# Kernel optimization log

Measured on AMD Instinct MI355X. Metric: run time of the kernel, lower is better.

Reference implementation:

```python
import jax, jax.numpy as jnp
import numpy as np

B, N, C, H, I, ID = 4, 1024, 1024, 16, 77, 768
HD = C // H
HID = 4 * C


def _ln(t, w, b):
    m = jnp.mean(t, axis=-1, keepdims=True)
    v = jnp.mean((t - m) ** 2, axis=-1, keepdims=True)
    return (t - m) * jax.lax.rsqrt(v + 1e-5) * w + b


def _gelu(t):
    return jax.nn.gelu(t, approximate=False)


def setup_inputs() -> dict:
    key = jax.random.key(0)
    ks = iter(jax.random.split(key, 16))

    def nrm(shape, s=0.02):
        return jax.random.normal(next(ks), shape, jnp.float32) * s

    return {
        'x': jax.random.normal(next(ks), (B, N, C), jnp.float32),
        'instruct_states': jax.random.normal(next(ks), (B, I, ID), jnp.float32),
        'norm1_w': jnp.ones((C,), jnp.float32), 'norm1_b': jnp.zeros((C,), jnp.float32),
        'qkv_w': nrm((3 * C, C)),
        'q_bias': jnp.zeros((C,), jnp.float32), 'v_bias': jnp.zeros((C,), jnp.float32),
        'proj_w': nrm((C, C)), 'proj_b': jnp.zeros((C,), jnp.float32),
        'gamma_1': jnp.full((C,), 1e-5, jnp.float32), 'gamma_2': jnp.full((C,), 1e-5, jnp.float32),
        'norm2_w': jnp.ones((C,), jnp.float32), 'norm2_b': jnp.zeros((C,), jnp.float32),
        'fc1_w': nrm((HID, C)), 'fc1_b': jnp.zeros((HID,), jnp.float32),
        'fc2_w': nrm((C, HID)), 'fc2_b': jnp.zeros((C,), jnp.float32),
        'pfc1_w': nrm((HID, C)), 'pfc1_b': jnp.zeros((HID,), jnp.float32),
        'pfc2_w': nrm((C, HID)), 'pfc2_b': jnp.zeros((C,), jnp.float32),
        'parallel_gate': jnp.full((1,), 0.1, jnp.float32),
        'ir_ln_w': jnp.ones((ID,), jnp.float32), 'ir_ln_b': jnp.zeros((ID,), jnp.float32),
        'ir_l1_w': nrm((C, ID)), 'ir_l1_b': jnp.zeros((C,), jnp.float32),
        'ir_l2_w': nrm((C, C)), 'ir_l2_b': jnp.zeros((C,), jnp.float32),
    }


def reference(x, instruct_states, norm1_w, norm1_b, qkv_w, q_bias, v_bias,
              proj_w, proj_b, gamma_1, gamma_2, norm2_w, norm2_b,
              fc1_w, fc1_b, fc2_w, fc2_b, pfc1_w, pfc1_b, pfc2_w, pfc2_b,
              parallel_gate, ir_ln_w, ir_ln_b, ir_l1_w, ir_l1_b, ir_l2_w, ir_l2_b):
    # instruct_dim_reduce: LN -> Linear -> GELU -> Linear
    kv = _ln(instruct_states, ir_ln_w, ir_ln_b)
    kv = _gelu(kv @ ir_l1_w.T + ir_l1_b) @ ir_l2_w.T + ir_l2_b  # [B, I, C]

    xn = _ln(x, norm1_w, norm1_b)                               # [B, N, C]
    cat = jnp.concatenate([kv, xn], axis=1)                     # [B, I+N, C]
    S = I + N

    qkv_bias = jnp.concatenate([q_bias, jnp.zeros_like(v_bias), v_bias])
    qkv = (cat @ qkv_w.T + qkv_bias).reshape(B, S, 3, H, HD)
    q = qkv[:, :, 0].transpose(0, 2, 1, 3)                      # [B, H, S, HD]
    k = qkv[:, :, 1].transpose(0, 2, 1, 3)
    v = qkv[:, :, 2].transpose(0, 2, 1, 3)

    # only visual queries, keys/values over instructions + visual tokens
    q = q[:, :, I:, :] * (HD ** -0.5)                           # [B, H, N, HD]
    attn = jnp.einsum('bhqd,bhkd->bhqk', q, k)                  # [B, H, N, S]
    attn = jax.nn.softmax(attn, axis=-1)
    o = jnp.einsum('bhqk,bhkd->bqhd', attn, v).reshape(B, N, C)
    o = o @ proj_w.T + proj_b

    x = x + gamma_1 * o                                         # LayerScale residual

    y = _ln(x, norm2_w, norm2_b)
    mlp = _gelu(y @ fc1_w.T + fc1_b) @ fc2_w.T + fc2_b
    pmlp = _gelu(y @ pfc1_w.T + pfc1_b) @ pfc2_w.T + pfc2_b
    x = x + gamma_2 * mlp + parallel_gate * pmlp
    return x
```

## Files before the change

### kernel.cpp

```cpp
#include <hip/hip_runtime.h>
#include <cstdint>

#define Bv   4
#define Nv   1024
#define Cv   1024
#define Hv   16
#define Iv   77
#define IDv  768
#define HDv  64
#define HIDv 4096
#define Sv   (Iv + Nv)
#define BIv  (Bv * Iv)
#define BSv  (Bv * Sv)
#define BNv  (Bv * Nv)
#define SPADv 1152

typedef __bf16 bf16x8_t __attribute__((ext_vector_type(8)));
typedef float  f32x4_t  __attribute__((ext_vector_type(4)));
typedef unsigned short us8_t __attribute__((ext_vector_type(8)));
typedef long  l2_t  __attribute__((ext_vector_type(2)));
typedef int   i32x4_t __attribute__((ext_vector_type(4)));
typedef int   i32x8_t __attribute__((ext_vector_type(8)));

__device__ inline f32x4_t zero4() { f32x4_t z; z[0]=0.f; z[1]=0.f; z[2]=0.f; z[3]=0.f; return z; }

__device__ inline unsigned short f2bf(float f) {
    unsigned int u = __builtin_bit_cast(unsigned int, f);
    u = (u + 0x7fffu + ((u >> 16) & 1u)) >> 16;
    return (unsigned short)u;
}
__device__ inline float bf2f(unsigned short u) {
    return __builtin_bit_cast(float, ((unsigned int)u) << 16);
}
__device__ inline unsigned int f4_fp8(float a, float b, float c, float d) {
    int v = __builtin_amdgcn_cvt_pk_fp8_f32(a, b, 0, false);
    v = __builtin_amdgcn_cvt_pk_fp8_f32(c, d, v, true);
    return (unsigned int)v;
}

__device__ inline float gelu_f(float x) {
    float u = 0.7978845608f * x * (1.0f + 0.044715f * x * x);
    float e = __expf(2.0f * u);
    float t = 1.0f - 2.0f / (e + 1.0f);
    return 0.5f * x * (1.0f + t);
}

__device__ inline void gload_lds16(const void* g, void* l) {
    __builtin_amdgcn_global_load_lds(
        (__attribute__((address_space(1))) void*)(unsigned long long)g,
        (__attribute__((address_space(3))) void*)(unsigned long long)l,
        16, 0, 0);
}

__device__ inline i32x8_t frag32(const unsigned char* p0, const unsigned char* p1) {
    i32x4_t lo = *(const i32x4_t*)p0;
    i32x4_t hi = *(const i32x4_t*)p1;
    i32x8_t r;
    r[0] = lo[0]; r[1] = lo[1]; r[2] = lo[2]; r[3] = lo[3];
    r[4] = hi[0]; r[5] = hi[1]; r[6] = hi[2]; r[7] = hi[3];
    return r;
}

#define PIPE_WAIT(N) do { \
    asm volatile("s_waitcnt vmcnt(" #N ")" ::: "memory"); \
    __builtin_amdgcn_s_barrier(); \
    __builtin_amdgcn_sched_barrier(0); \
} while (0)
#define PIPE_RELEASE() do { \
    __builtin_amdgcn_sched_barrier(0); \
    __builtin_amdgcn_s_barrier(); \
} while (0)

__global__ __launch_bounds__(256) void cvt8_kernel(
        const float* s0, const float* s1, const float* s2, const float* s3,
        const float* s4, const float* s5, const float* s6, const float* s7,
        void* d0, void* d1, void* d2, void* d3,
        void* d4, void* d5, void* d6, void* d7,
        const float* g1, const float* g2, const float* gate) {
    (void)g1;
    long i = (long)blockIdx.x * 256 + threadIdx.x;
    const float* src; void* dst; long off;
    const float* sptr = nullptr; int K4 = 1; float wmul = 1.0f; bool f8 = false;
    if (i < 2097152) {
        if (i < 786432)       { src = s0; dst = d0; off = i; f8 = true; wmul = 32.f; }
        else if (i < 1048576) { src = s1; dst = d1; off = i - 786432;  f8 = true; wmul = 32.f; }
        else                  { src = s2; dst = d2; off = i - 1048576; f8 = true; wmul = 32.f; }
    } else if (i < 4194304) {
        if (i < 3145728)      { src = s3; dst = d3; off = i - 2097152; f8 = true; wmul = 32.f; sptr = g2; K4 = 1024; }
        else                  { src = s4; dst = d4; off = i - 3145728; f8 = true; wmul = 32.f; }
    } else {
        if (i < 5242880)      { src = s5; dst = d5; off = i - 4194304; f8 = true; wmul = 32.f; sptr = gate; K4 = 0x7fffffff; }
        else if (i < 5439488) { src = s6; dst = d6; off = i - 5242880; }
        else                  { src = s7; dst = d7; off = i - 5439488; }
    }
    float sc = (sptr ? sptr[(int)(off / K4)] : 1.0f) * wmul;
    float4 v = ((const float4*)src)[off];
    if (f8) {
        ((unsigned int*)dst)[off] = f4_fp8(v.x * sc, v.y * sc, v.z * sc, v.w * sc);
    } else {
        ushort4 o = {f2bf(v.x * sc), f2bf(v.y * sc), f2bf(v.z * sc), f2bf(v.w * sc)};
        ((ushort4*)dst)[off] = o;
    }
}

__global__ __launch_bounds__(256) void bias_prep_kernel(
        const float* __restrict__ qb, const float* __restrict__ vb,
        const float* __restrict__ fc2b, const float* __restrict__ pfc2b,
        const float* __restrict__ projb_in,
        const float* __restrict__ fc1b, const float* __restrict__ pfc1b,
        const float* __restrict__ g1, const float* __restrict__ g2,
        const float* __restrict__ gate,
        float* __restrict__ qkvb, float* __restrict__ bfuse,
        float* __restrict__ projb, float* __restrict__ bcat) {
    int i = blockIdx.x * 256 + threadIdx.x;
    if (i < 3 * Cv) {
        float v = 0.f;
        if (i < Cv) v = qb[i];
        else if (i >= 2 * Cv) v = vb[i - 2 * Cv];
        qkvb[i] = v;
    } else if (i < 4 * Cv) {
        int n = i - 3 * Cv;
        bfuse[n] = g2[n] * fc2b[n] + gate[0] * pfc2b[n];
    } else if (i < 5 * Cv) {
        int n = i - 4 * Cv;
        projb[n] = g1[n] * projb_in[n];
    } else if (i < 13 * Cv) {
        int j = i - 5 * Cv;
        bcat[j] = (j < HIDv) ? fc1b[j] : pfc1b[j - HIDv];
    }
}

__global__ __launch_bounds__(256) void scatter_kv_kernel(const unsigned short* __restrict__ kv,
                                                         unsigned char* __restrict__ cat) {
    int r = blockIdx.x;
    int b = r / Iv, i = r % Iv;
    const ushort4* src = (const ushort4*)(kv + (size_t)r * Cv);
    unsigned int* dst = (unsigned int*)(cat + (size_t)(b * Sv + i) * Cv);
    ushort4 u = src[threadIdx.x];
    dst[threadIdx.x] = f4_fp8(bf2f(u.x) * 16.f, bf2f(u.y) * 16.f,
                              bf2f(u.z) * 16.f, bf2f(u.w) * 16.f);
}

template <int F8>
__global__ __launch_bounds__(256) void ln_kernel(const float* __restrict__ in,
                                                 const float* __restrict__ w,
                                                 const float* __restrict__ bvec,
                                                 void* __restrict__ out,
                                                 int cols, float invcols,
                                                 int div_, int stride_, int off_) {
    const int r = blockIdx.x;
    const int tid = threadIdx.x;
    const float* row = in + (size_t)r * cols;
    float s = 0.f, s2 = 0.f;
    for (int c = tid * 4; c < cols; c += 1024) {
        float4 v = *(const float4*)(row + c);
        s  += v.x + v.y + v.z + v.w;
        s2 += v.x * v.x + v.y * v.y + v.z * v.z + v.w * v.w;
    }
#pragma unroll
    for (int o2 = 32; o2 > 0; o2 >>= 1) { s += __shfl_down(s, o2); s2 += __shfl_down(s2, o2); }
    __shared__ float sh[10];
    const int lane = tid & 63, wave = tid >> 6;
    if (lane == 0) { sh[wave] = s; sh[4 + wave] = s2; }
    __syncthreads();
    if (tid == 0) {
        float S1 = sh[0] + sh[1] + sh[2] + sh[3];
        float S2 = sh[4] + sh[5] + sh[6] + sh[7];
        float mean = S1 * invcols;
        float var  = S2 * invcols - mean * mean;
        sh[8] = mean;
        sh[9] = rsqrtf(var + 1e-5f);
    }
    __syncthreads();
    const float mean = sh[8], rstd = sh[9];
    const size_t orow = (size_t)((r / div_) * stride_ + (r % div_) + off_) * cols;
    for (int c = tid * 4; c < cols; c += 1024) {
        float4 v  = *(const float4*)(row + c);
        float4 wv = *(const float4*)(w + c);
        float4 bv = *(const float4*)(bvec + c);
        float o0 = (v.x - mean) * rstd * wv.x + bv.x;
        float o1 = (v.y - mean) * rstd * wv.y + bv.y;
        float o2 = (v.z - mean) * rstd * wv.z + bv.z;
        float o3 = (v.w - mean) * rstd * wv.w + bv.w;
        if constexpr (F8) {
            *(unsigned int*)((unsigned char*)out + orow + c) =
                f4_fp8(o0 * 16.f, o1 * 16.f, o2 * 16.f, o3 * 16.f);
        } else {
            ushort4 o = {f2bf(o0), f2bf(o1), f2bf(o2), f2bf(o3)};
            *(ushort4*)((unsigned short*)out + orow + c) = o;
        }
    }
}

template <int MODE>
__global__ __launch_bounds__(256) void gemm_bf16_kernel(
        const unsigned short* __restrict__ A,
        const unsigned short* __restrict__ W,
        const float* __restrict__ bias,
        unsigned short* __restrict__ outp,
        int M, int N, int K) {
    __shared__ unsigned short As[2][128 * 32];
    __shared__ unsigned short Bs[2][128 * 32];
    const int tid  = threadIdx.x;
    const int lane = tid & 63;
    const int wave = tid >> 6;
    const int m16  = lane & 15;
    const int g4   = lane >> 4;
    const int n0 = blockIdx.x * 128;
    const int m0 = blockIdx.y * 128;
    const int wm = (wave >> 1) * 64;
    const int wn = (wave & 1) * 64;

    const int r0  = tid >> 2;
    const int cc0 = (tid & 3) * 8;
    int am0 = m0 + r0;       if (am0 > M - 1) am0 = M - 1;
    int am1 = m0 + r0 + 64;  if (am1 > M - 1) am1 = M - 1;
    const unsigned short* agp0 = A + (size_t)am0 * K + cc0;
    const unsigned short* agp1 = A + (size_t)am1 * K + cc0;
    const unsigned short* bgp0 = W + (size_t)(n0 + r0) * K + cc0;
    const unsigned short* bgp1 = W + (size_t)(n0 + r0 + 64) * K + cc0;

    f32x4_t acc[4][4];
#pragma unroll
    for (int a = 0; a < 4; ++a)
#pragma unroll
        for (int bb = 0; bb < 4; ++bb) acc[a][bb] = zero4();

    auto stage = [&](int buf) {
        gload_lds16(agp0, &As[buf][wave * 512]);
        gload_lds16(agp1, &As[buf][2048 + wave * 512]);
        gload_lds16(bgp0, &Bs[buf][wave * 512]);
        gload_lds16(bgp1, &Bs[buf][2048 + wave * 512]);
        agp0 += 32; agp1 += 32; bgp0 += 32; bgp1 += 32;
    };

    auto body = [&](int cur) {
        bf16x8_t xf[4], wf[4];
#pragma unroll
        for (int bb = 0; bb < 4; ++bb)
            xf[bb] = *(const bf16x8_t*)&As[cur][(wm + bb * 16 + m16) * 32 + g4 * 8];
#pragma unroll
        for (int a = 0; a < 4; ++a)
            wf[a] = *(const bf16x8_t*)&Bs[cur][(wn + a * 16 + m16) * 32 + g4 * 8];
#pragma unroll
        for (int a = 0; a < 4; ++a)
#pragma unroll
            for (int bb = 0; bb < 4; ++bb)
                acc[a][bb] = __builtin_amdgcn_mfma_f32_16x16x32_bf16(wf[a], xf[bb], acc[a][bb], 0, 0, 0);
    };

    const int NIT = K >> 5;
    stage(0);
    stage(1);
    for (int it = 0; it < NIT - 1; ++it) {
        const int cur = it & 1;
        PIPE_WAIT(4);
        body(cur);
        PIPE_RELEASE();
        if (it + 2 < NIT) stage(cur);
    }
    PIPE_WAIT(0);
    body((NIT - 1) & 1);

#pragma unroll
    for (int a = 0; a < 4; ++a) {
        const int cb = n0 + wn + a * 16 + g4 * 4;
        const float4 bv4 = *(const float4*)(bias + cb);
#pragma unroll
        for (int bb = 0; bb < 4; ++bb) {
            const int r = m0 + wm + bb * 16 + m16;
            if (r < M) {
                const size_t idx = (size_t)r * N + cb;
                const float v0 = acc[a][bb][0] + bv4.x;
                const float v1 = acc[a][bb][1] + bv4.y;
                const float v2 = acc[a][bb][2] + bv4.z;
                const float v3 = acc[a][bb][3] + bv4.w;
                if constexpr (MODE == 0) {
                    ushort4 o = {f2bf(v0), f2bf(v1), f2bf(v2), f2bf(v3)};
                    *(ushort4*)(outp + idx) = o;
                } else {
                    ushort4 o = {f2bf(gelu_f(v0)), f2bf(gelu_f(v1)),
                                 f2bf(gelu_f(v2)), f2bf(gelu_f(v3))};
                    *(ushort4*)(outp + idx) = o;
                }
            }
        }
    }
}

__global__ __launch_bounds__(256) void gemm_fp8_bf16out_kernel(
        const unsigned char* __restrict__ A,
        const unsigned char* __restrict__ W,
        const float* __restrict__ bias,
        unsigned short* __restrict__ outp,
        int M, int N, int K) {
    __shared__ unsigned char As[2][128 * 128];
    __shared__ unsigned char Bs[2][128 * 128];
    const int tid  = threadIdx.x;
    const int lane = tid & 63;
    const int wave = tid >> 6;
    const int m16  = lane & 15;
    const int g4   = lane >> 4;
    const int n0 = blockIdx.x * 128;
    const int m0 = blockIdx.y * 128;
    const int wm = (wave >> 1) * 64;
    const int wn = (wave & 1) * 64;

    const int rowin = tid >> 3;
    const int sslot = (tid & 7) ^ (rowin & 7);
    const unsigned char* agp[4];
#pragma unroll
    for (int j = 0; j < 4; ++j) {
        int gr = m0 + j * 32 + rowin; if (gr > M - 1) gr = M - 1;
        agp[j] = A + (size_t)gr * K + sslot * 16;
    }
    const unsigned char* bgp = W + (size_t)(n0 + rowin) * K + sslot * 16;

    const int sw = m16 & 7;
    const int ra0 = ((2 * g4) ^ sw) * 16;
    const int ra1 = ((2 * g4 + 1) ^ sw) * 16;

    f32x4_t acc[4][4];
#pragma unroll
    for (int a = 0; a < 4; ++a)
#pragma unroll
        for (int bb = 0; bb < 4; ++bb) acc[a][bb] = zero4();

    auto stage = [&](int buf) {
#pragma unroll
        for (int j = 0; j < 4; ++j) {
            gload_lds16(agp[j], &As[buf][j * 4096 + wave * 1024]);
            gload_lds16(bgp + (size_t)j * 32 * K, &Bs[buf][j * 4096 + wave * 1024]);
            agp[j] += 128;
        }
        bgp += 128;
    };

    stage(0);
    const int NIT = K >> 7;
    for (int it = 0; it < NIT; ++it) {
        const int cur = it & 1;
        __syncthreads();
        if (it + 1 < NIT) stage(cur ^ 1);
        i32x8_t xv[4], wv[4];
#pragma unroll
        for (int bb = 0; bb < 4; ++bb) {
            const unsigned char* rb = &As[cur][(wm + bb * 16 + m16) * 128];
            xv[bb] = frag32(rb + ra0, rb + ra1);
        }
#pragma unroll
        for (int a = 0; a < 4; ++a) {
            const unsigned char* rb = &Bs[cur][(wn + a * 16 + m16) * 128];
            wv[a] = frag32(rb + ra0, rb + ra1);
        }
#pragma unroll
        for (int a = 0; a < 4; ++a)
#pragma unroll
            for (int bb = 0; bb < 4; ++bb)
                acc[a][bb] = __builtin_amdgcn_mfma_scale_f32_16x16x128_f8f6f4(
                    wv[a], xv[bb], acc[a][bb], 0, 0, 0, 0x7f7f7f7f, 0, 0x7f7f7f7f);
    }

    const float ds = 1.0f / 512.0f;
#pragma unroll
    for (int a = 0; a < 4; ++a) {
        const int cb = n0 + wn + a * 16 + g4 * 4;
        const float4 bv4 = *(const float4*)(bias + cb);
#pragma unroll
        for (int bb = 0; bb < 4; ++bb) {
            const int r = m0 + wm + bb * 16 + m16;
            if (r < M) {
                const size_t idx = (size_t)r * N + cb;
                ushort4 o = {f2bf(acc[a][bb][0] * ds + bv4.x),
                             f2bf(acc[a][bb][1] * ds + bv4.y),
                             f2bf(acc[a][bb][2] * ds + bv4.z),
                             f2bf(acc[a][bb][3] * ds + bv4.w)};
                *(ushort4*)(outp + idx) = o;
            }
        }
    }
}

__global__ __launch_bounds__(256) void gemm_fp8_gelu_kernel(
        const unsigned char* __restrict__ A,
        const unsigned char* __restrict__ W,
        const float* __restrict__ bias,
        unsigned char* __restrict__ outp,
        int M, int N, int K) {
    __shared__ unsigned char As[2][128 * 128];
    __shared__ unsigned char Bs[2][128 * 128];
    const int tid  = threadIdx.x;
    const int lane = tid & 63;
    const int wave = tid >> 6;
    const int m16  = lane & 15;
    const int g4   = lane >> 4;
    const int bid = blockIdx.x;
    const int xcd = bid & 7, l = bid >> 3;
    const int by = (xcd << 2) | (l & 3);
    const int bx = l >> 2;
    const int n0 = bx * 128;
    const int m0 = by * 128;
    const int wm = (wave >> 1) * 64;
    const int wn = (wave & 1) * 64;

    const int rowin = tid >> 3;
    const int sslot = (tid & 7) ^ (rowin & 7);
    const unsigned char* agp = A + (size_t)(m0 + rowin) * K + sslot * 16;
    const unsigned char* bgp = W + (size_t)(n0 + rowin) * K + sslot * 16;

    const int sw = m16 & 7;
    const int ra0 = ((2 * g4) ^ sw) * 16;
    const int ra1 = ((2 * g4 + 1) ^ sw) * 16;

    f32x4_t acc[4][4];
#pragma unroll
    for (int a = 0; a < 4; ++a)
#pragma unroll
        for (int bb = 0; bb < 4; ++bb) acc[a][bb] = zero4();

    auto stage = [&](int buf) {
#pragma unroll
        for (int j = 0; j < 4; ++j) {
            gload_lds16(agp + (size_t)j * 32 * K, &As[buf][j * 4096 + wave * 1024]);
            gload_lds16(bgp + (size_t)j * 32 * K, &Bs[buf][j * 4096 + wave * 1024]);
        }
        agp += 128; bgp += 128;
    };

    stage(0);
    const int NIT = K >> 7;
    for (int it = 0; it < NIT; ++it) {
        const int cur = it & 1;
        __syncthreads();
        if (it + 1 < NIT) stage(cur ^ 1);
        i32x8_t xv[4], wv[4];
#pragma unroll
        for (int bb = 0; bb < 4; ++bb) {
            const unsigned char* rb = &As[cur][(wm + bb * 16 + m16) * 128];
            xv[bb] = frag32(rb + ra0, rb + ra1);
        }
#pragma unroll
        for (int a = 0; a < 4; ++a) {
            const unsigned char* rb = &Bs[cur][(wn + a * 16 + m16) * 128];
            wv[a] = frag32(rb + ra0, rb + ra1);
        }
#pragma unroll
        for (int a = 0; a < 4; ++a)
#pragma unroll
            for (int bb = 0; bb < 4; ++bb)
                acc[a][bb] = __builtin_amdgcn_mfma_scale_f32_16x16x128_f8f6f4(
                    wv[a], xv[bb], acc[a][bb], 0, 0, 0, 0x7f7f7f7f, 0, 0x7f7f7f7f);
    }

    const float ds = 1.0f / 512.0f;
#pragma unroll
    for (int a = 0; a < 4; ++a) {
        const int cb = n0 + wn + a * 16 + g4 * 4;
        const float4 bv4 = *(const float4*)(bias + cb);
#pragma unroll
        for (int bb = 0; bb < 4; ++bb) {
            const int r = m0 + wm + bb * 16 + m16;
            const size_t idx = (size_t)r * N + cb;
            unsigned int pk = f4_fp8(gelu_f(acc[a][bb][0] * ds + bv4.x) * 16.f,
                                     gelu_f(acc[a][bb][1] * ds + bv4.y) * 16.f,
                                     gelu_f(acc[a][bb][2] * ds + bv4.z) * 16.f,
                                     gelu_f(acc[a][bb][3] * ds + bv4.w) * 16.f);
            *(unsigned int*)(outp + idx) = pk;
        }
    }
}

__global__ __launch_bounds__(256) void gemm_fp8_splitk_kernel(
        const unsigned char* __restrict__ A1,
        const unsigned char* __restrict__ W1,
        const unsigned char* __restrict__ A2,
        const unsigned char* __restrict__ W2,
        unsigned short* __restrict__ parts,
        int M, int N, int lda, int ldw, int Kc, int zsplit) {
    __shared__ unsigned char As[2][128 * 128];
    __shared__ unsigned char Bs[2][128 * 128];
    const int tid  = threadIdx.x;
    const int lane = tid & 63;
    const int wave = tid >> 6;
    const int m16  = lane & 15;
    const int g4   = lane >> 4;
    const int bid = blockIdx.x;
    const int xcd = bid & 7, l = bid >> 3;
    const int by = (xcd << 2) | (l & 3);
    const int rr = l >> 2;
    const int bx = rr & 7;
    const int z  = rr >> 3;
    const int n0 = bx * 128;
    const int m0 = by * 128;
    const int wm = (wave >> 1) * 64;
    const int wn = (wave & 1) * 64;

    const unsigned char* A = (z < zsplit) ? A1 : A2;
    const unsigned char* W = (z < zsplit) ? W1 : W2;
    const int k0 = (z % zsplit) * Kc;

    const int rowin = tid >> 3;
    const int sslot = (tid & 7) ^ (rowin & 7);
    const unsigned char* agp = A + (size_t)(m0 + rowin) * lda + k0 + sslot * 16;
    const unsigned char* bgp = W + (size_t)(n0 + rowin) * ldw + k0 + sslot * 16;

    const int sw = m16 & 7;
    const int ra0 = ((2 * g4) ^ sw) * 16;
    const int ra1 = ((2 * g4 + 1) ^ sw) * 16;

    f32x4_t acc[4][4];
#pragma unroll
    for (int a = 0; a < 4; ++a)
#pragma unroll
        for (int bb = 0; bb < 4; ++bb) acc[a][bb] = zero4();

    auto stage = [&](int buf) {
#pragma unroll
        for (int j = 0; j < 4; ++j) {
            gload_lds16(agp + (size_t)j * 32 * lda, &As[buf][j * 4096 + wave * 1024]);
            gload_lds16(bgp + (size_t)j * 32 * ldw, &Bs[buf][j * 4096 + wave * 1024]);
        }
        agp += 128; bgp += 128;
    };

    stage(0);
    const int NIT = Kc >> 7;
    for (int it = 0; it < NIT; ++it) {
        const int cur = it & 1;
        __syncthreads();
        if (it + 1 < NIT) stage(cur ^ 1);
        i32x8_t xv[4], wv[4];
#pragma unroll
        for (int bb = 0; bb < 4; ++bb) {
            const unsigned char* rb = &As[cur][(wm + bb * 16 + m16) * 128];
            xv[bb] = frag32(rb + ra0, rb + ra1);
        }
#pragma unroll
        for (int a = 0; a < 4; ++a) {
            const unsigned char* rb = &Bs[cur][(wn + a * 16 + m16) * 128];
            wv[a] = frag32(rb + ra0, rb + ra1);
        }
#pragma unroll
        for (int a = 0; a < 4; ++a)
#pragma unroll
            for (int bb = 0; bb < 4; ++bb)
                acc[a][bb] = __builtin_amdgcn_mfma_scale_f32_16x16x128_f8f6f4(
                    wv[a], xv[bb], acc[a][bb], 0, 0, 0, 0x7f7f7f7f, 0, 0x7f7f7f7f);
    }

    unsigned short* pz = parts + (size_t)z * M * N;
    const float ds = 1.0f / 512.0f;
#pragma unroll
    for (int a = 0; a < 4; ++a) {
        const int cb = n0 + wn + a * 16 + g4 * 4;
#pragma unroll
        for (int bb = 0; bb < 4; ++bb) {
            const int r = m0 + wm + bb * 16 + m16;
            const size_t idx = (size_t)r * N + cb;
            ushort4 o = {f2bf(acc[a][bb][0] * ds), f2bf(acc[a][bb][1] * ds),
                         f2bf(acc[a][bb][2] * ds), f2bf(acc[a][bb][3] * ds)};
            *(ushort4*)(pz + idx) = o;
        }
    }
}

template <int NP>
__global__ __launch_bounds__(256) void reduce_kernel(
        const unsigned short* __restrict__ parts,
        const float* __restrict__ resid,
        const float* __restrict__ bias,
        float* __restrict__ out, int MN, int N4mask) {
    int i = blockIdx.x * 256 + threadIdx.x;
    if (i * 4 >= MN) return;
    float4 res = ((const float4*)resid)[i];
    float4 bv  = *(const float4*)(bias + (i & N4mask) * 4);
    float4 o = {res.x + bv.x, res.y + bv.y, res.z + bv.z, res.w + bv.w};
#pragma unroll
    for (int z = 0; z < NP; ++z) {
        ushort4 u = ((const ushort4*)(parts + (size_t)z * MN))[i];
        o.x += bf2f(u.x); o.y += bf2f(u.y); o.z += bf2f(u.z); o.w += bf2f(u.w);
    }
    ((float4*)out)[i] = o;
}

template <int NP>
__global__ __launch_bounds__(256) void reduce_scale_kernel(
        const unsigned short* __restrict__ parts,
        const float* __restrict__ resid,
        const float* __restrict__ bias,
        const float* __restrict__ scale,
        float* __restrict__ out, int MN, int N4mask) {
    int i = blockIdx.x * 256 + threadIdx.x;
    if (i * 4 >= MN) return;
    float4 res = ((const float4*)resid)[i];
    const int c4 = (i & N4mask) * 4;
    float4 bv = *(const float4*)(bias + c4);
    float4 sc = *(const float4*)(scale + c4);
    float sx = 0.f, sy = 0.f, sz = 0.f, sw = 0.f;
#pragma unroll
    for (int z = 0; z < NP; ++z) {
        ushort4 u = ((const ushort4*)(parts + (size_t)z * MN))[i];
        sx += bf2f(u.x); sy += bf2f(u.y); sz += bf2f(u.z); sw += bf2f(u.w);
    }
    float4 o = {res.x + bv.x + sc.x * sx, res.y + bv.y + sc.y * sy,
                res.z + bv.z + sc.z * sz, res.w + bv.w + sc.w * sw};
    ((float4*)out)[i] = o;
}

__global__ __launch_bounds__(256) void vtrans_kernel(const unsigned short* __restrict__ qkv,
                                                     unsigned short* __restrict__ vt) {
    __shared__ unsigned short Vs[64 * 64];
    const int stile = blockIdx.x;
    const int bh = blockIdx.y;
    const int b = bh >> 4, h = bh & 15;
    const int tid = threadIdx.x;
#pragma unroll
    for (int j = 0; j < 2; ++j) {
        int c = j * 256 + tid;
        int r = c >> 3, d8 = (c & 7) * 8;
        int s = stile * 64 + r;
        uint4 v = {0u, 0u, 0u, 0u};
        if (s < Sv) v = *(const uint4*)(qkv + ((size_t)(b * Sv + s) * 3 + 2) * Cv + h * 64 + d8);
        *(uint4*)&Vs[r * 64 + d8] = v;
    }
    __syncthreads();
    const int d  = tid >> 2;
    const int p0 = (tid & 3) * 16;
    unsigned short tmp[16];
#pragma unroll
    for (int e = 0; e < 16; ++e) {
        int p = p0 + e;
        int s_local = (p & 32) + 16 * ((p >> 2) & 1) + 4 * ((p & 31) >> 3) + (p & 3);
        tmp[e] = Vs[s_local * 64 + d];
    }
    unsigned short* dst = vt + ((size_t)bh * 64 + d) * SPADv + stile * 64 + p0;
    *(uint4*)dst       = *(const uint4*)&tmp[0];
    *(uint4*)(dst + 8) = *(const uint4*)&tmp[8];
}

__global__ __launch_bounds__(256) void attn_kernel(const unsigned short* __restrict__ qkv,
                                                   const unsigned short* __restrict__ vt,
                                                   unsigned char* __restrict__ o) {
    __shared__ unsigned short Qs[64 * 64];
    __shared__ unsigned short Ks[2][64 * 64];
    __shared__ unsigned short Vts[2][64 * 64];

    const int tid  = threadIdx.x;
    const int lane = tid & 63;
    const int wave = tid >> 6;
    const int m16  = lane & 15;
    const int g4   = lane >> 4;
    const int qt = blockIdx.x;
    const int bh = blockIdx.y;
    const int b = bh >> 4, h = bh & 15;

    const int lr = lane >> 3;
    const int csw = ((lane & 7) ^ lr) * 8;
    const int sw7 = m16 & 7;

#pragma unroll
    for (int j = 0; j < 2; ++j) {
        int r = wave * 16 + j * 8 + lr;
        int s = Iv + qt * 64 + r;
        gload_lds16(qkv + ((size_t)(b * Sv + s) * 3) * Cv + h * 64 + csw,
                    &Qs[(wave * 16 + j * 8) * 64]);
    }

    auto stage_kv = [&](int st, int buf) {
#pragma unroll
        for (int j = 0; j < 2; ++j) {
            int r = wave * 16 + j * 8 + lr;
            int s = st * 64 + r; if (s > Sv - 1) s = Sv - 1;
            gload_lds16(qkv + ((size_t)(b * Sv + s) * 3 + 1) * Cv + h * 64 + csw,
                        &Ks[buf][(wave * 16 + j * 8) * 64]);
            gload_lds16(vt + ((size_t)bh * 64 + r) * SPADv + st * 64 + csw,
                        &Vts[buf][(wave * 16 + j * 8) * 64]);
        }
    };

    f32x4_t oacc[4];
#pragma unroll
    for (int dt = 0; dt < 4; ++dt) oacc[dt] = zero4();
    float m_run = -1e30f, l_run = 0.f;

    stage_kv(0, 0);
    __syncthreads();

    const bf16x8_t qf0 = *(const bf16x8_t*)&Qs[(wave * 16 + m16) * 64 + ((g4 ^ sw7) * 8)];
    const bf16x8_t qf1 = *(const bf16x8_t*)&Qs[(wave * 16 + m16) * 64 + (((4 + g4) ^ sw7) * 8)];

    const int NT = (Sv + 63) / 64;
    for (int st = 0; st < NT; ++st) {
        const int cur = st & 1;
        if (st + 1 < NT) stage_kv(st + 1, cur ^ 1);

        f32x4_t sc[4];
#pragma unroll
        for (int kt = 0; kt < 4; ++kt) {
            bf16x8_t k0 = *(const bf16x8_t*)&Ks[cur][(kt * 16 + m16) * 64 + ((g4 ^ sw7) * 8)];
            bf16x8_t k1 = *(const bf16x8_t*)&Ks[cur][(kt * 16 + m16) * 64 + (((4 + g4) ^ sw7) * 8)];
            f32x4_t z = zero4();
            z = __builtin_amdgcn_mfma_f32_16x16x32_bf16(k0, qf0, z, 0, 0, 0);
            z = __builtin_amdgcn_mfma_f32_16x16x32_bf16(k1, qf1, z, 0, 0, 0);
            sc[kt] = z;
        }

        float mx = -1e30f;
#pragma unroll
        for (int kt = 0; kt < 4; ++kt)
#pragma unroll
            for (int r = 0; r < 4; ++r) {
                int key = st * 64 + kt * 16 + g4 * 4 + r;
                float v = sc[kt][r] * 0.125f;
                v = (key < Sv) ? v : -1e30f;
                sc[kt][r] = v;
                mx = fmaxf(mx, v);
            }
        mx = fmaxf(mx, __shfl_xor(mx, 16));
        mx = fmaxf(mx, __shfl_xor(mx, 32));
        const float mnew  = fmaxf(m_run, mx);
        const float alpha = __expf(m_run - mnew);
        m_run = mnew;
        float sum = 0.f;
#pragma unroll
        for (int kt = 0; kt < 4; ++kt)
#pragma unroll
            for (int r = 0; r < 4; ++r) {
                float p = __expf(sc[kt][r] - mnew);
                sc[kt][r] = p;
                sum += p;
            }
        sum += __shfl_xor(sum, 16);
        sum += __shfl_xor(sum, 32);
        l_run = l_run * alpha + sum;
#pragma unroll
        for (int dt = 0; dt < 4; ++dt) oacc[dt] *= alpha;

        us8_t pu0, pu1;
#pragma unroll
        for (int j = 0; j < 8; ++j) {
            pu0[j] = f2bf(sc[(j >> 2)][j & 3]);
            pu1[j] = f2bf(sc[2 + (j >> 2)][j & 3]);
        }
        const bf16x8_t pf0 = __builtin_bit_cast(bf16x8_t, pu0);
        const bf16x8_t pf1 = __builtin_bit_cast(bf16x8_t, pu1);

#pragma unroll
        for (int dt = 0; dt < 4; ++dt) {
            bf16x8_t v0 = *(const bf16x8_t*)&Vts[cur][(dt * 16 + m16) * 64 + ((g4 ^ sw7) * 8)];
            bf16x8_t v1 = *(const bf16x8_t*)&Vts[cur][(dt * 16 + m16) * 64 + (((4 + g4) ^ sw7) * 8)];
            oacc[dt] = __builtin_amdgcn_mfma_f32_16x16x32_bf16(v0, pf0, oacc[dt], 0, 0, 0);
            oacc[dt] = __builtin_amdgcn_mfma_f32_16x16x32_bf16(v1, pf1, oacc[dt], 0, 0, 0);
        }
        __syncthreads();
    }

    const float inv16 = 16.0f / l_run;
    const int q = qt * 64 + wave * 16 + m16;
    const size_t row = (size_t)(b * Nv + q) * Cv + h * 64;
#pragma unroll
    for (int dt = 0; dt < 4; ++dt) {
        *(unsigned int*)&o[row + dt * 16 + g4 * 4] =
            f4_fp8(oacc[dt][0] * inv16, oacc[dt][1] * inv16,
                   oacc[dt][2] * inv16, oacc[dt][3] * inv16);
    }
}

extern "C" void kernel_launch(void* const* d_in, const int* in_sizes, int n_in,
                              void* d_out, int out_size, void* d_ws, size_t ws_size,
                              hipStream_t stream) {
    (void)in_sizes; (void)n_in; (void)out_size; (void)ws_size;
    const float* x       = (const float*)d_in[0];
    const float* instr   = (const float*)d_in[1];
    const float* norm1_w = (const float*)d_in[2];
    const float* norm1_b = (const float*)d_in[3];
    const float* qkv_w   = (const float*)d_in[4];
    const float* q_bias  = (const float*)d_in[5];
    const float* v_bias  = (const float*)d_in[6];
    const float* proj_w  = (const float*)d_in[7];
    const float* proj_b  = (const float*)d_in[8];
    const float* gamma_1 = (const float*)d_in[9];
    const float* gamma_2 = (const float*)d_in[10];
    const float* norm2_w = (const float*)d_in[11];
    const float* norm2_b = (const float*)d_in[12];
    const float* fc1_w   = (const float*)d_in[13];
    const float* fc1_b   = (const float*)d_in[14];
    const float* fc2_w   = (const float*)d_in[15];
    const float* fc2_b   = (const float*)d_in[16];
    const float* pfc1_w  = (const float*)d_in[17];
    const float* pfc1_b  = (const float*)d_in[18];
    const float* pfc2_w  = (const float*)d_in[19];
    const float* pfc2_b  = (const float*)d_in[20];
    const float* gate    = (const float*)d_in[21];
    const float* ir_ln_w = (const float*)d_in[22];
    const float* ir_ln_b = (const float*)d_in[23];
    const float* ir_l1_w = (const float*)d_in[24];
    const float* ir_l1_b = (const float*)d_in[25];
    const float* ir_l2_w = (const float*)d_in[26];
    const float* ir_l2_b = (const float*)d_in[27];
    float* out = (float*)d_out;

    char* ws = (char*)d_ws;
    size_t off = 0;
    auto alloc = [&](size_t bytes) -> char* {
        char* p = ws + off;
        off += (bytes + 255) & ~(size_t)255;
        return p;
    };
    unsigned char*  w_qkv8 = (unsigned char*)alloc((size_t)3 * Cv * Cv);
    unsigned char*  w_proj8= (unsigned char*)alloc((size_t)Cv * Cv);
    unsigned char*  w_mlp1 = (unsigned char*)alloc((size_t)2 * HIDv * Cv);
    unsigned char*  w_fc2  = (unsigned char*)alloc((size_t)Cv * HIDv);
    unsigned char*  w_pfc2 = (unsigned char*)alloc((size_t)Cv * HIDv);
    unsigned short* w_ir1  = (unsigned short*)alloc((size_t)Cv * IDv * 2);
    unsigned short* w_ir2  = (unsigned short*)alloc((size_t)Cv * Cv * 2);
    float*          qkvb   = (float*)alloc((size_t)3 * Cv * 4);
    float*          bfuse  = (float*)alloc((size_t)Cv * 4);
    float*          projb  = (float*)alloc((size_t)Cv * 4);
    float*          bcat   = (float*)alloc((size_t)2 * HIDv * 4);
    unsigned short* irln   = (unsigned short*)alloc((size_t)BIv * IDv * 2);
    unsigned short* h1     = (unsigned short*)alloc((size_t)BIv * Cv * 2);
    unsigned short* kvtmp  = (unsigned short*)alloc((size_t)BIv * Cv * 2);
    unsigned char*  cat8   = (unsigned char*)alloc((size_t)BSv * Cv);
    unsigned short* qkvbuf = (unsigned short*)alloc((size_t)BSv * 3 * Cv * 2);
    unsigned char*  obuf8  = (unsigned char*)alloc((size_t)BNv * Cv);
    float*          x1     = (float*)alloc((size_t)BNv * Cv * 4);
    unsigned char*  ybuf8  = (unsigned char*)alloc((size_t)BNv * Cv);
    unsigned char*  gbufA  = (unsigned char*)alloc((size_t)BNv * 2 * HIDv);
    unsigned short* fpart  = (unsigned short*)alloc((size_t)4 * BNv * Cv * 2);
    unsigned short* vt     = (unsigned short*)gbufA;
    unsigned short* ppart  = fpart;

    cvt8_kernel<<<22272, 256, 0, stream>>>(qkv_w, proj_w, fc1_w, fc2_w, pfc1_w, pfc2_w,
                                           ir_l1_w, ir_l2_w,
                                           w_qkv8, w_proj8, w_mlp1, w_fc2,
                                           w_mlp1 + (size_t)HIDv * Cv, w_pfc2,
                                           w_ir1, w_ir2,
                                           gamma_1, gamma_2, gate);

    bias_prep_kernel<<<52, 256, 0, stream>>>(q_bias, v_bias, fc2_b, pfc2_b, proj_b,
                                             fc1_b, pfc1_b,
                                             gamma_1, gamma_2, gate,
                                             qkvb, bfuse, projb, bcat);

    ln_kernel<0><<<BIv, 256, 0, stream>>>(instr, ir_ln_w, ir_ln_b, irln,
                                          IDv, 1.0f / IDv, 1 << 28, 0, 0);
    ln_kernel<1><<<BNv, 256, 0, stream>>>(x, norm1_w, norm1_b, cat8,
                                          Cv, 1.0f / Cv, Nv, Sv, Iv);
    gemm_bf16_kernel<1><<<dim3(Cv / 128, (BIv + 127) / 128), 256, 0, stream>>>(
        irln, w_ir1, ir_l1_b, h1, BIv, Cv, IDv);
    gemm_bf16_kernel<0><<<dim3(Cv / 128, (BIv + 127) / 128), 256, 0, stream>>>(
        h1, w_ir2, ir_l2_b, kvtmp, BIv, Cv, Cv);
    scatter_kv_kernel<<<BIv, 256, 0, stream>>>(kvtmp, cat8);

    gemm_fp8_bf16out_kernel<<<dim3(3 * Cv / 128, (BSv + 127) / 128), 256, 0, stream>>>(
        cat8, w_qkv8, qkvb, qkvbuf, BSv, 3 * Cv, Cv);

    vtrans_kernel<<<dim3(18, Bv * Hv), 256, 0, stream>>>(qkvbuf, vt);
    attn_kernel<<<dim3(Nv / 64, Bv * Hv), 256, 0, stream>>>(qkvbuf, vt, obuf8);

    gemm_fp8_splitk_kernel<<<1024, 256, 0, stream>>>(
        obuf8, w_proj8, obuf8, w_proj8, ppart,
        BNv, Cv, Cv, Cv, Cv / 4, 4);
    reduce_scale_kernel<4><<<(BNv * Cv / 4 + 255) / 256, 256, 0, stream>>>(
        ppart, x, projb, gamma_1, x1, BNv * Cv, Cv / 4 - 1);

    ln_kernel<1><<<BNv, 256, 0, stream>>>(x1, norm2_w, norm2_b, ybuf8,
                                          Cv, 1.0f / Cv, 1 << 28, 0, 0);

    gemm_fp8_gelu_kernel<<<2048, 256, 0, stream>>>(
        ybuf8, w_mlp1, bcat, gbufA, BNv, 2 * HIDv, Cv);

    gemm_fp8_splitk_kernel<<<1024, 256, 0, stream>>>(
        gbufA, w_fc2, gbufA + HIDv, w_pfc2, fpart,
        BNv, Cv, 2 * HIDv, HIDv, HIDv / 2, 2);
    reduce_kernel<4><<<(BNv * Cv / 4 + 255) / 256, 256, 0, stream>>>(
        fpart, x1, bfuse, out, BNv * Cv, Cv / 4 - 1);
}
```

Before: 436.8 us.

## Fuse proj reduce with LN2, fold kv scatter into GEMM, halve split-K

A new kernel combines the proj split-K partial reduction, residual add and the second LayerNorm into one pass. It writes x1 in fp32 and y in fp8 together, so x1 is no longer re-read from global memory. The instruct-reduce second GEMM gains an epilogue mode that writes fp8 rows straight into the concatenated buffer, which removes the temporary buffer and the scatter kernel. Split-K counts drop from 4 to 2 for both the proj and fc2 GEMMs, with half the launched blocks, which cuts partial-sum traffic but may lower parallelism. The LN variance now uses E[x²]-mean², which is less numerically stable.

```diff
diff --git a/kernel.cpp b/kernel.cpp
--- a/kernel.cpp
+++ b/kernel.cpp
@@ -130,17 +130,6 @@
     }
 }
 
-__global__ __launch_bounds__(256) void scatter_kv_kernel(const unsigned short* __restrict__ kv,
-                                                         unsigned char* __restrict__ cat) {
-    int r = blockIdx.x;
-    int b = r / Iv, i = r % Iv;
-    const ushort4* src = (const ushort4*)(kv + (size_t)r * Cv);
-    unsigned int* dst = (unsigned int*)(cat + (size_t)(b * Sv + i) * Cv);
-    ushort4 u = src[threadIdx.x];
-    dst[threadIdx.x] = f4_fp8(bf2f(u.x) * 16.f, bf2f(u.y) * 16.f,
-                              bf2f(u.z) * 16.f, bf2f(u.w) * 16.f);
-}
-
 template <int F8>
 __global__ __launch_bounds__(256) void ln_kernel(const float* __restrict__ in,
                                                  const float* __restrict__ w,
@@ -190,6 +179,56 @@
             *(ushort4*)((unsigned short*)out + orow + c) = o;
         }
     }
+}
+
+__global__ __launch_bounds__(256) void proj_ln2_kernel(
+        const unsigned short* __restrict__ parts,
+        const float* __restrict__ x,
+        const float* __restrict__ projb,
+        const float* __restrict__ g1,
+        const float* __restrict__ w, const float* __restrict__ bvec,
+        float* __restrict__ x1, unsigned char* __restrict__ y8) {
+    const int r = blockIdx.x;
+    const int tid = threadIdx.x;
+    const int c = tid * 4;
+    const size_t base = (size_t)r * Cv + c;
+    float4 xv = *(const float4*)(x + base);
+    float4 pb = *(const float4*)(projb + c);
+    float4 gv = *(const float4*)(g1 + c);
+    ushort4 u0 = *(const ushort4*)(parts + base);
+    ushort4 u1 = *(const ushort4*)(parts + (size_t)BNv * Cv + base);
+    float4 v;
+    v.x = xv.x + pb.x + gv.x * (bf2f(u0.x) + bf2f(u1.x));
+    v.y = xv.y + pb.y + gv.y * (bf2f(u0.y) + bf2f(u1.y));
+    v.z = xv.z + pb.z + gv.z * (bf2f(u0.z) + bf2f(u1.z));
+    v.w = xv.w + pb.w + gv.w * (bf2f(u0.w) + bf2f(u1.w));
+    *(float4*)(x1 + base) = v;
+
+    float s  = v.x + v.y + v.z + v.w;
+    float s2 = v.x * v.x + v.y * v.y + v.z * v.z + v.w * v.w;
+#pragma unroll
+    for (int o2 = 32; o2 > 0; o2 >>= 1) { s += __shfl_down(s, o2); s2 += __shfl_down(s2, o2); }
+    __shared__ float sh[10];
+    const int lane = tid & 63, wave = tid >> 6;
+    if (lane == 0) { sh[wave] = s; sh[4 + wave] = s2; }
+    __syncthreads();
+    if (tid == 0) {
+        float S1 = sh[0] + sh[1] + sh[2] + sh[3];
+        float S2 = sh[4] + sh[5] + sh[6] + sh[7];
+        float mean = S1 * (1.0f / Cv);
+        float var  = S2 * (1.0f / Cv) - mean * mean;
+        sh[8] = mean;
+        sh[9] = rsqrtf(var + 1e-5f);
+    }
+    __syncthreads();
+    const float mean = sh[8], rstd = sh[9];
+    float4 wv = *(const float4*)(w + c);
+    float4 bv = *(const float4*)(bvec + c);
+    float o0 = (v.x - mean) * rstd * wv.x + bv.x;
+    float o1 = (v.y - mean) * rstd * wv.y + bv.y;
+    float o2 = (v.z - mean) * rstd * wv.z + bv.z;
+    float o3 = (v.w - mean) * rstd * wv.w + bv.w;
+    *(unsigned int*)(y8 + base) = f4_fp8(o0 * 16.f, o1 * 16.f, o2 * 16.f, o3 * 16.f);
 }
 
 template <int MODE>
@@ -270,18 +309,23 @@
         for (int bb = 0; bb < 4; ++bb) {
             const int r = m0 + wm + bb * 16 + m16;
             if (r < M) {
-                const size_t idx = (size_t)r * N + cb;
                 const float v0 = acc[a][bb][0] + bv4.x;
                 const float v1 = acc[a][bb][1] + bv4.y;
                 const float v2 = acc[a][bb][2] + bv4.z;
                 const float v3 = acc[a][bb][3] + bv4.w;
                 if constexpr (MODE == 0) {
+                    const size_t idx = (size_t)r * N + cb;
                     ushort4 o = {f2bf(v0), f2bf(v1), f2bf(v2), f2bf(v3)};
                     *(ushort4*)(outp + idx) = o;
-                } else {
+                } else if constexpr (MODE == 1) {
+                    const size_t idx = (size_t)r * N + cb;
                     ushort4 o = {f2bf(gelu_f(v0)), f2bf(gelu_f(v1)),
                                  f2bf(gelu_f(v2)), f2bf(gelu_f(v3))};
                     *(ushort4*)(outp + idx) = o;
+                } else {
+                    const int rr2 = (r / Iv) * Sv + (r % Iv);
+                    *(unsigned int*)((unsigned char*)outp + (size_t)rr2 * Cv + cb) =
+                        f4_fp8(v0 * 16.f, v1 * 16.f, v2 * 16.f, v3 * 16.f);
                 }
             }
         }
@@ -580,30 +624,6 @@
         ushort4 u = ((const ushort4*)(parts + (size_t)z * MN))[i];
         o.x += bf2f(u.x); o.y += bf2f(u.y); o.z += bf2f(u.z); o.w += bf2f(u.w);
     }
-    ((float4*)out)[i] = o;
-}
-
-template <int NP>
-__global__ __launch_bounds__(256) void reduce_scale_kernel(
-        const unsigned short* __restrict__ parts,
-        const float* __restrict__ resid,
-        const float* __restrict__ bias,
-        const float* __restrict__ scale,
-        float* __restrict__ out, int MN, int N4mask) {
-    int i = blockIdx.x * 256 + threadIdx.x;
-    if (i * 4 >= MN) return;
-    float4 res = ((const float4*)resid)[i];
-    const int c4 = (i & N4mask) * 4;
-    float4 bv = *(const float4*)(bias + c4);
-    float4 sc = *(const float4*)(scale + c4);
-    float sx = 0.f, sy = 0.f, sz = 0.f, sw = 0.f;
-#pragma unroll
-    for (int z = 0; z < NP; ++z) {
-        ushort4 u = ((const ushort4*)(parts + (size_t)z * MN))[i];
-        sx += bf2f(u.x); sy += bf2f(u.y); sz += bf2f(u.z); sw += bf2f(u.w);
-    }
-    float4 o = {res.x + bv.x + sc.x * sx, res.y + bv.y + sc.y * sy,
-                res.z + bv.z + sc.z * sz, res.w + bv.w + sc.w * sw};
     ((float4*)out)[i] = o;
 }
 
@@ -820,14 +840,13 @@
     float*          bcat   = (float*)alloc((size_t)2 * HIDv * 4);
     unsigned short* irln   = (unsigned short*)alloc((size_t)BIv * IDv * 2);
     unsigned short* h1     = (unsigned short*)alloc((size_t)BIv * Cv * 2);
-    unsigned short* kvtmp  = (unsigned short*)alloc((size_t)BIv * Cv * 2);
     unsigned char*  cat8   = (unsigned char*)alloc((size_t)BSv * Cv);
     unsigned short* qkvbuf = (unsigned short*)alloc((size_t)BSv * 3 * Cv * 2);
     unsigned char*  obuf8  = (unsigned char*)alloc((size_t)BNv * Cv);
     float*          x1     = (float*)alloc((size_t)BNv * Cv * 4);
     unsigned char*  ybuf8  = (unsigned char*)alloc((size_t)BNv * Cv);
     unsigned char*  gbufA  = (unsigned char*)alloc((size_t)BNv * 2 * HIDv);
-    unsigned short* fpart  = (unsigned short*)alloc((size_t)4 * BNv * Cv * 2);
+    unsigned short* fpart  = (unsigned short*)alloc((size_t)2 * BNv * Cv * 2);
     unsigned short* vt     = (unsigned short*)gbufA;
     unsigned short* ppart  = fpart;
 
@@ -849,9 +868,8 @@
                                           Cv, 1.0f / Cv, Nv, Sv, Iv);
     gemm_bf16_kernel<1><<<dim3(Cv / 128, (BIv + 127) / 128), 256, 0, stream>>>(
         irln, w_ir1, ir_l1_b, h1, BIv, Cv, IDv);
-    gemm_bf16_kernel<0><<<dim3(Cv / 128, (BIv + 127) / 128), 256, 0, stream>>>(
-        h1, w_ir2, ir_l2_b, kvtmp, BIv, Cv, Cv);
-    scatter_kv_kernel<<<BIv, 256, 0, stream>>>(kvtmp, cat8);
+    gemm_bf16_kernel<2><<<dim3(Cv / 128, (BIv + 127) / 128), 256, 0, stream>>>(
+        h1, w_ir2, ir_l2_b, (unsigned short*)cat8, BIv, Cv, Cv);
 
     gemm_fp8_bf16out_kernel<<<dim3(3 * Cv / 128, (BSv + 127) / 128), 256, 0, stream>>>(
         cat8, w_qkv8, qkvb, qkvbuf, BSv, 3 * Cv, Cv);
@@ -859,21 +877,18 @@
     vtrans_kernel<<<dim3(18, Bv * Hv), 256, 0, stream>>>(qkvbuf, vt);
     attn_kernel<<<dim3(Nv / 64, Bv * Hv), 256, 0, stream>>>(qkvbuf, vt, obuf8);
 
-    gemm_fp8_splitk_kernel<<<1024, 256, 0, stream>>>(
+    gemm_fp8_splitk_kernel<<<512, 256, 0, stream>>>(
         obuf8, w_proj8, obuf8, w_proj8, ppart,
-        BNv, Cv, Cv, Cv, Cv / 4, 4);
-    reduce_scale_kernel<4><<<(BNv * Cv / 4 + 255) / 256, 256, 0, stream>>>(
-        ppart, x, projb, gamma_1, x1, BNv * Cv, Cv / 4 - 1);
-
-    ln_kernel<1><<<BNv, 256, 0, stream>>>(x1, norm2_w, norm2_b, ybuf8,
-                                          Cv, 1.0f / Cv, 1 << 28, 0, 0);
+        BNv, Cv, Cv, Cv, Cv / 2, 2);
+    proj_ln2_kernel<<<BNv, 256, 0, stream>>>(
+        ppart, x, projb, gamma_1, norm2_w, norm2_b, x1, ybuf8);
 
     gemm_fp8_gelu_kernel<<<2048, 256, 0, stream>>>(
         ybuf8, w_mlp1, bcat, gbufA, BNv, 2 * HIDv, Cv);
 
-    gemm_fp8_splitk_kernel<<<1024, 256, 0, stream>>>(
+    gemm_fp8_splitk_kernel<<<512, 256, 0, stream>>>(
         gbufA, w_fc2, gbufA + HIDv, w_pfc2, fpart,
-        BNv, Cv, 2 * HIDv, HIDv, HIDv / 2, 2);
-    reduce_kernel<4><<<(BNv * Cv / 4 + 255) / 256, 256, 0, stream>>>(
+        BNv, Cv, 2 * HIDv, HIDv, HIDv, 1);
+    reduce_kernel<2><<<(BNv * Cv / 4 + 255) / 256, 256, 0, stream>>>(
         fpart, x1, bfuse, out, BNv * Cv, Cv / 4 - 1);
 }
```

New measurement: 438.7 us. Within noise of the previous version (+0.4%).
